# Kernel tuning notes

Measured on AMD Instinct MI355X. Metric: run time of the kernel, lower is better.

Reference implementation:

```python
import jax, jax.numpy as jnp
import numpy as np

QMIN, QMAX = -128, 127  # signed int8 range


def setup_inputs() -> dict:
    key = jax.random.key(0)
    k_x, k_w, k_b = jax.random.split(key, 3)
    N, C_in, H, W = 32, 128, 56, 56
    C_out, kH, kW = 256, 3, 3
    # int8-valued tensors carried as int32 (jax-friendly); values in [-128, 127]
    x = jax.random.randint(k_x, (N, C_in, H, W), 0, 256, dtype=jnp.int32) - 128
    weight = jax.random.randint(k_w, (C_out, C_in, kH, kW), 0, 256, dtype=jnp.int32) - 128
    # int32 bias, already quantized with scale s_in * s_w
    bias = jax.random.randint(k_b, (C_out,), -(2 ** 14), 2 ** 14, dtype=jnp.int32)
    return {
        "x": x,
        "weight": weight,
        "bias": bias,
        "input_scale": jnp.float32(0.02),
        "weight_scale": jnp.float32(0.005),
        "output_scale": jnp.float32(0.05),
        "input_zero_point": jnp.int32(-5),
        "output_zero_point": jnp.int32(3),
    }


def reference(x, weight, bias, input_scale, weight_scale, output_scale,
              input_zero_point, output_zero_point):
    # Dequant-style integer conv: shift input by its zero point (weights are
    # symmetric, zero point 0), accumulate in fp32 (stands in for int32 acc).
    x_f = (x - input_zero_point).astype(jnp.float32)
    w_f = weight.astype(jnp.float32)
    acc = jax.lax.conv_general_dilated(
        x_f, w_f,
        window_strides=(1, 1),
        padding=((1, 1), (1, 1)),
        dimension_numbers=("NCHW", "OIHW", "NCHW"),
    )
    acc = acc + bias.astype(jnp.float32)[None, :, None, None]
    # Requantize: scale fusion + output zero point, round, clamp to int8.
    requant_scale = input_scale * weight_scale / output_scale
    y = acc * requant_scale + output_zero_point.astype(jnp.float32)
    y_q = jnp.clip(jnp.round(y), QMIN, QMAX).astype(jnp.int8)
    return y_q
```

## Files before the change

kernel.cpp:

```cpp
#include <hip/hip_runtime.h>
#include <stdint.h>


#define NB 32
#define CI 128
#define HH 56
#define WW 56
#define CO 256
#define SPA (HH * WW)
#define HP 58
#define WP 64
#define XP2_BYTES (NB * HP * WP * CI)
#define BP_BYTES (9 * 2 * 4 * CO * 16)
#define ABUF (4 * 8192)

typedef int v4i __attribute__((ext_vector_type(4)));

__global__ __launch_bounds__(256) void prep_kernel(
    const int* __restrict__ x, const int* __restrict__ wgt,
    const int* __restrict__ bias, const int* __restrict__ zpi,
    int8_t* __restrict__ xp2, int8_t* __restrict__ bp, int* __restrict__ BG)
{
    __shared__ int sm[1824];
    const int tid = threadIdx.x, bid = blockIdx.x;
    const int zp = *zpi;
    const int zp4 = (zp & 255) * 0x01010101;

    if (bid < HH * NB) {
        const int n = bid / HH, h = bid % HH;
        #pragma unroll
        for (int it = 0; it < 7; ++it) {
            int j = tid + it * 256;
            int ci = j / 14, w4 = j - ci * 14;
            const v4i v = *(const v4i*)(x + ((n * CI + ci) * HH + h) * WW + w4 * 4);
            sm[w4 * 130 + ci] = (v.x & 255) | ((v.y & 255) << 8) |
                                ((v.z & 255) << 16) | (v.w << 24);
        }
        __syncthreads();
        int* od = (int*)xp2 + (n * HP + h + 1) * (WP * CI / 4);
        #pragma unroll
        for (int it = 0; it < 8; ++it) {
            int j = tid + it * 256;
            int widx = j >> 5, ci4 = j & 31;
            int val = zp4;
            if (widx >= 1 && widx <= WW) {
                int w = widx - 1;
                int base = (w >> 2) * 130 + ci4 * 4;
                int sh = (w & 3) * 8;
                val = ((sm[base] >> sh) & 0xff) | (((sm[base+1] >> sh) & 0xff) << 8) |
                      (((sm[base+2] >> sh) & 0xff) << 16) | ((sm[base+3] >> sh) << 24);
            }
            od[j ^ ((widx & 7) << 2)] = val;
        }
    } else if (bid < HH * NB + 2 * NB) {
        const int z = bid - HH * NB;
        const int n = z >> 1, hidx = (z & 1) ? (HP - 1) : 0;
        int* od = (int*)xp2 + (n * HP + hidx) * (WP * CI / 4);
        #pragma unroll
        for (int it = 0; it < 8; ++it) od[tid + it * 256] = zp4;
    } else {
        const int co = bid - (HH * NB + 2 * NB);
        for (int j = tid; j < 1152; j += 256) sm[j] = wgt[co * 1152 + j];
        __syncthreads();
        for (int j = tid; j < 288; j += 256) {
            int j4 = j & 3, q = (j >> 2) & 3, c64 = (j >> 4) & 1, t = j >> 5;
            int ci = c64 * 64 + q * 16 + j4 * 4;
            int b0 = sm[(ci + 0) * 9 + t] & 255, b1 = sm[(ci + 1) * 9 + t] & 255;
            int b2 = sm[(ci + 2) * 9 + t] & 255, b3 = sm[(ci + 3) * 9 + t];
            ((int*)bp)[((t * 2 + c64) * 4 + q) * 1024 + co * 4 + j4] =
                b0 | (b1 << 8) | (b2 << 16) | (b3 << 24);
        }
        if (tid < 9) {
            int s = 0;
            for (int ci = 0; ci < CI; ++ci) s += sm[ci * 9 + tid];
            sm[1152 + tid] = s;
        }
        __syncthreads();
        if (tid == 0) {
            int s9 = 0;
            for (int t = 0; t < 9; ++t) s9 += sm[1152 + t];
            BG[co] = bias[co] - zp * s9;
        }
    }
}

__global__ __launch_bounds__(128)
__attribute__((amdgpu_waves_per_eu(2)))
void qconv_mfma(
    const int8_t* __restrict__ xp2, const int8_t* __restrict__ bp,
    const int* __restrict__ BG,
    const float* __restrict__ si, const float* __restrict__ sw,
    const float* __restrict__ so, const int* __restrict__ zpo,
    int* __restrict__ out)
{
    const int tid  = threadIdx.x, lane = tid & 63, wid = tid >> 6;
    const int quad = lane >> 4, lo16 = lane & 15;
    const int bid  = blockIdx.x;
    const int xcd  = bid & 7, idx = bid >> 3;
    const int n    = xcd * 4 + (idx & 3);
    const int cb   = (idx >> 2) & 1;
    const int s2   = idx >> 3;
    const int cw   = cb * 128 + wid * 64;

    __shared__ __attribute__((aligned(16))) int8_t Asm[ABUF];

    const int8_t* src0 = xp2 + (((size_t)n * HP + 2 * s2) << 13);
    #pragma unroll
    for (int k = 0; k < 16; ++k) {
        const int u = wid + 2 * k;
        __builtin_amdgcn_global_load_lds(
            (const __attribute__((address_space(1))) void*)(src0 + (u << 10) + lane * 16),
            (__attribute__((address_space(3))) void*)(&Asm[u << 10]), 16, 0, 0);
    }

    int bgv[4];
    #pragma unroll
    for (int ct = 0; ct < 4; ++ct) bgv[ct] = BG[cw + ct * 16 + lo16];
    const float rs = (*si) * (*sw) / (*so);
    const float zo = (float)(*zpo);

    int boff[7];
    #pragma unroll
    for (int mt = 0; mt < 7; ++mt) {
        const int ml = mt * 16 + lo16;
        const int srow = ml / 56, scol = ml - srow * 56;
        boff[mt] = srow * 8192 + scol * 128 + quad * 16;
    }

    const int8_t* bwav = bp + ((size_t)quad << 12) + ((cw + lo16) << 4);

    int* optr = out + ((size_t)n * CO + cw + lo16) * SPA + quad * 4;

    #define BLOAD(tp) {                                                        \
        const int8_t* bb = bwav + ((tp) * 8 << 12);                            \
        asm volatile("" : "+v"(bb));                                           \
        bt[(tp) & 1][0] = *(const v4i*)(bb);                                   \
        bt[(tp) & 1][1] = *(const v4i*)(bb + 256);                             \
        bt[(tp) & 1][2] = *(const v4i*)(bb + 512);                             \
        bt[(tp) & 1][3] = *(const v4i*)(bb + 768);                             \
        bt[(tp) & 1][4] = *(const v4i*)(bb + 16384);                           \
        bt[(tp) & 1][5] = *(const v4i*)(bb + 16384 + 256);                     \
        bt[(tp) & 1][6] = *(const v4i*)(bb + 16384 + 512);                     \
        bt[(tp) & 1][7] = *(const v4i*)(bb + 16384 + 768);                     \
    }

    #define AADDR(tp, mt) ({                                                   \
        const int off_ = boff[mt] + ((tp) / 3) * 8192 + ((tp) % 3) * 128;      \
        off_ ^ (((off_ >> 7) & 7) << 4); })

    v4i bt[2][8];
    BLOAD(0);

    v4i acc[7][4];
    #pragma unroll
    for (int mt = 0; mt < 7; ++mt)
        #pragma unroll
        for (int ct = 0; ct < 4; ++ct) acc[mt][ct] = (v4i){0, 0, 0, 0};

    __syncthreads();

    v4i a0p[2], a1p[2];
    { const int p = AADDR(0, 0);
      a0p[0] = *(const v4i*)(Asm + p); a1p[0] = *(const v4i*)(Asm + (p ^ 64)); }

    #pragma unroll
    for (int it = 0; it < 63; ++it) {
        const int tp = it / 7, mt = it % 7;
        if (mt == 0 && tp + 1 <= 8) BLOAD(tp + 1);
        if (it + 1 < 63) {
            const int p = AADDR((it + 1) / 7, (it + 1) % 7);
            a0p[(it + 1) & 1] = *(const v4i*)(Asm + p);
            a1p[(it + 1) & 1] = *(const v4i*)(Asm + (p ^ 64));
        }
        const v4i a0 = a0p[it & 1], a1 = a1p[it & 1];
        #pragma unroll
        for (int ct = 0; ct < 4; ++ct)
            acc[mt][ct] = __builtin_amdgcn_mfma_i32_16x16x64_i8(a0, bt[tp & 1][ct], acc[mt][ct], 0, 0, 0);
        #pragma unroll
        for (int ct = 0; ct < 4; ++ct)
            acc[mt][ct] = __builtin_amdgcn_mfma_i32_16x16x64_i8(a1, bt[tp & 1][4 + ct], acc[mt][ct], 0, 0, 0);
    }
    #undef BLOAD
    #undef AADDR

    const int m0 = s2 * 112;
    #pragma unroll
    for (int mt = 0; mt < 7; ++mt) {
        #pragma unroll
        for (int ct = 0; ct < 4; ++ct) {
            v4i vv;
            #pragma unroll
            for (int i4 = 0; i4 < 4; ++i4) {
                float yv = rintf((float)(acc[mt][ct][i4] + bgv[ct]) * rs + zo);
                yv = fminf(fmaxf(yv, -128.f), 127.f);
                vv[i4] = (int)yv;
            }
            *(v4i*)(optr + ct * 16 * SPA + m0 + mt * 16) = vv;
        }
    }
}

extern "C" void kernel_launch(void* const* d_in, const int* in_sizes, int n_in,
                              void* d_out, int out_size, void* d_ws, size_t ws_size,
                              hipStream_t stream) {
    const int*   x    = (const int*)d_in[0];
    const int*   wgt  = (const int*)d_in[1];
    const int*   bias = (const int*)d_in[2];
    const float* si   = (const float*)d_in[3];
    const float* sw   = (const float*)d_in[4];
    const float* so   = (const float*)d_in[5];
    const int*   zpi  = (const int*)d_in[6];
    const int*   zpo  = (const int*)d_in[7];
    int* out = (int*)d_out;

    int8_t* xp2 = (int8_t*)d_ws;
    int8_t* bp  = xp2 + XP2_BYTES;
    int*    bg  = (int*)(bp + BP_BYTES);

    prep_kernel<<<HH * NB + 2 * NB + CO, 256, 0, stream>>>(x, wgt, bias, zpi, xp2, bp, bg);
    qconv_mfma<<<1792, 128, 0, stream>>>(xp2, bp, bg, si, sw, so, zpo, out);
}
```

Baseline: 191.3 us.

## Drop LDS staging; read A tiles directly from global in single-wave blocks

The conv kernel no longer stages the input tile into shared memory with global_load_lds and a barrier. Each single-wave block now loads A fragments straight from global memory with a 3-deep register prefetch, and the grid doubles to 3584 blocks of 64 threads. This removes the LDS copy and block-wide sync and should raise occupancy. In exchange, the A data is no longer shared across waves through LDS, so every fragment load goes to global memory or cache with higher latency, and cache traffic roughly doubles.

```diff
diff --git a/kernel.cpp b/kernel.cpp
--- a/kernel.cpp
+++ b/kernel.cpp
@@ -12,7 +12,6 @@
 #define WP 64
 #define XP2_BYTES (NB * HP * WP * CI)
 #define BP_BYTES (9 * 2 * 4 * CO * 16)
-#define ABUF (4 * 8192)
 
 typedef int v4i __attribute__((ext_vector_type(4)));
 
@@ -84,34 +83,23 @@
     }
 }
 
-__global__ __launch_bounds__(128)
-__attribute__((amdgpu_waves_per_eu(2)))
-void qconv_mfma(
+__global__ __launch_bounds__(64) void qconv_mfma(
     const int8_t* __restrict__ xp2, const int8_t* __restrict__ bp,
     const int* __restrict__ BG,
     const float* __restrict__ si, const float* __restrict__ sw,
     const float* __restrict__ so, const int* __restrict__ zpo,
     int* __restrict__ out)
 {
-    const int tid  = threadIdx.x, lane = tid & 63, wid = tid >> 6;
+    const int lane = threadIdx.x & 63;
     const int quad = lane >> 4, lo16 = lane & 15;
     const int bid  = blockIdx.x;
     const int xcd  = bid & 7, idx = bid >> 3;
     const int n    = xcd * 4 + (idx & 3);
-    const int cb   = (idx >> 2) & 1;
-    const int s2   = idx >> 3;
-    const int cw   = cb * 128 + wid * 64;
-
-    __shared__ __attribute__((aligned(16))) int8_t Asm[ABUF];
-
-    const int8_t* src0 = xp2 + (((size_t)n * HP + 2 * s2) << 13);
-    #pragma unroll
-    for (int k = 0; k < 16; ++k) {
-        const int u = wid + 2 * k;
-        __builtin_amdgcn_global_load_lds(
-            (const __attribute__((address_space(1))) void*)(src0 + (u << 10) + lane * 16),
-            (__attribute__((address_space(3))) void*)(&Asm[u << 10]), 16, 0, 0);
-    }
+    const int co64 = (idx >> 2) & 3;
+    const int s2   = idx >> 4;
+    const int cw   = co64 * 64;
+
+    const int8_t* ag = xp2 + (((size_t)n * HP + 2 * s2) << 13);
 
     int bgv[4];
     #pragma unroll
@@ -157,22 +145,22 @@
         #pragma unroll
         for (int ct = 0; ct < 4; ++ct) acc[mt][ct] = (v4i){0, 0, 0, 0};
 
-    __syncthreads();
-
-    v4i a0p[2], a1p[2];
+    v4i a0p[3], a1p[3];
     { const int p = AADDR(0, 0);
-      a0p[0] = *(const v4i*)(Asm + p); a1p[0] = *(const v4i*)(Asm + (p ^ 64)); }
+      a0p[0] = *(const v4i*)(ag + p); a1p[0] = *(const v4i*)(ag + (p ^ 64)); }
+    { const int p = AADDR(0, 1);
+      a0p[1] = *(const v4i*)(ag + p); a1p[1] = *(const v4i*)(ag + (p ^ 64)); }
 
     #pragma unroll
     for (int it = 0; it < 63; ++it) {
         const int tp = it / 7, mt = it % 7;
         if (mt == 0 && tp + 1 <= 8) BLOAD(tp + 1);
-        if (it + 1 < 63) {
-            const int p = AADDR((it + 1) / 7, (it + 1) % 7);
-            a0p[(it + 1) & 1] = *(const v4i*)(Asm + p);
-            a1p[(it + 1) & 1] = *(const v4i*)(Asm + (p ^ 64));
-        }
-        const v4i a0 = a0p[it & 1], a1 = a1p[it & 1];
+        if (it + 2 < 63) {
+            const int p = AADDR((it + 2) / 7, (it + 2) % 7);
+            a0p[(it + 2) % 3] = *(const v4i*)(ag + p);
+            a1p[(it + 2) % 3] = *(const v4i*)(ag + (p ^ 64));
+        }
+        const v4i a0 = a0p[it % 3], a1 = a1p[it % 3];
         #pragma unroll
         for (int ct = 0; ct < 4; ++ct)
             acc[mt][ct] = __builtin_amdgcn_mfma_i32_16x16x64_i8(a0, bt[tp & 1][ct], acc[mt][ct], 0, 0, 0);
@@ -218,5 +206,5 @@
     int*    bg  = (int*)(bp + BP_BYTES);
 
     prep_kernel<<<HH * NB + 2 * NB + CO, 256, 0, stream>>>(x, wgt, bias, zpi, xp2, bp, bg);
-    qconv_mfma<<<1792, 128, 0, stream>>>(xp2, bp, bg, si, sw, so, zpo, out);
+    qconv_mfma<<<3584, 64, 0, stream>>>(xp2, bp, bg, si, sw, so, zpo, out);
 }
```

After: 197.6 us. +3.3%, slower.
